# Performance work log

Measured on AMD Instinct MI355X. Metric: run time of the kernel, lower is better.

Reference implementation:

```python
import jax, jax.numpy as jnp
import numpy as np

NUM_EMBEDDINGS = 1024
EMBEDDING_DIM = 256
COMMITMENT_COST = 0.25


def setup_inputs() -> dict:
    key = jax.random.key(0)
    k1, k2 = jax.random.split(key)
    inputs = jax.random.normal(k1, (64, 32, 32, EMBEDDING_DIM), dtype=jnp.float32)
    embed = jax.random.normal(k2, (NUM_EMBEDDINGS, EMBEDDING_DIM), dtype=jnp.float32)
    return {"inputs": inputs, "embed": embed}


def reference(inputs, embed):
    # Eval-mode forward (no EMA buffer mutation), use_ema=True loss branch.
    input_shape = inputs.shape
    flat = inputs.reshape(-1, EMBEDDING_DIM)  # [N, d]
    distances = (
        jnp.sum(flat * flat, axis=1, keepdims=True)
        + jnp.sum(embed * embed, axis=1)
        - 2.0 * jnp.matmul(flat, embed.T)
    )
    encoding_indices = jnp.argmin(distances, axis=1)  # [N]
    # Gather codebook rows (equivalent to one-hot @ embed)
    quantized = embed[encoding_indices].reshape(input_shape)
    # use_ema branch: loss = commitment * mse(stop_grad(quantized), inputs)
    e_latent_loss = jnp.mean((jax.lax.stop_gradient(quantized) - inputs) ** 2)
    loss = COMMITMENT_COST * e_latent_loss
    # Straight-through estimator
    quantized_st = inputs + jax.lax.stop_gradient(quantized - inputs)
    # Perplexity from code usage histogram (== mean of one-hot encodings)
    n_tokens = flat.shape[0]
    counts = jax.ops.segment_sum(
        jnp.ones((n_tokens,), dtype=jnp.float32), encoding_indices,
        num_segments=NUM_EMBEDDINGS)
    avg_probs = counts / n_tokens
    perplexity = jnp.exp(-jnp.sum(avg_probs * jnp.log(avg_probs + 1e-10)))
    return quantized_st, loss, perplexity, encoding_indices
```

## Files before the change

kernel.cpp:

```cpp
#include <hip/hip_runtime.h>

#define NTOK 65536
#define DIM 256
#define KC 1024
#define EPS 0.08f

typedef __attribute__((ext_vector_type(8))) _Float16 f16x8;
typedef __attribute__((ext_vector_type(8))) unsigned short u16x8;
typedef __attribute__((ext_vector_type(4))) float f32x4;

static __device__ __forceinline__ unsigned short f16bits(float f) {
  _Float16 h = (_Float16)f;
  return __builtin_bit_cast(unsigned short, h);
}

#define VWAIT(n) asm volatile("s_waitcnt vmcnt(" #n ")" ::: "memory")
#define SB() __builtin_amdgcn_sched_barrier(0)
#define GLDX4(dst, p, off) \
  asm volatile("global_load_dwordx4 %0, %1, off offset:" #off \
               : "=v"(dst) : "v"(p) : "memory")

__global__ __launch_bounds__(256) void vq_prep_e(const float* __restrict__ e,
                                                 unsigned short* __restrict__ eg,
                                                 float* __restrict__ esq,
                                                 int* __restrict__ hist,
                                                 int* __restrict__ fixCount) {
  const int gid = blockIdx.x * 256 + threadIdx.x;
  const int t = gid >> 5;
  const int o = gid & 31;
  const float4 v0 = *reinterpret_cast<const float4*>(&e[t * DIM + o * 8]);
  const float4 v1 = *reinterpret_cast<const float4*>(&e[t * DIM + o * 8 + 4]);
  u16x8 u;
  u[0] = f16bits(v0.x); u[1] = f16bits(v0.y); u[2] = f16bits(v0.z); u[3] = f16bits(v0.w);
  u[4] = f16bits(v1.x); u[5] = f16bits(v1.y); u[6] = f16bits(v1.z); u[7] = f16bits(v1.w);
  const int ctk = t >> 6, njj = (t >> 4) & 3, col = t & 15;
  const int s = o >> 2, kq = o & 3;
  char* dst = (char*)eg + ((ctk * 32 + s * 4 + njj) << 10) + ((kq * 16 + col) << 4);
  *reinterpret_cast<u16x8*>(dst) = u;
  float p = v0.x * v0.x + v0.y * v0.y + v0.z * v0.z + v0.w * v0.w +
            v1.x * v1.x + v1.y * v1.y + v1.z * v1.z + v1.w * v1.w;
#pragma unroll
  for (int m = 16; m > 0; m >>= 1) p += __shfl_xor(p, m, 64);
  if (o == 0) esq[t] = p;
  if (blockIdx.x < 4) hist[blockIdx.x * 256 + threadIdx.x] = 0;
  if (gid == 0) *fixCount = 0;
}

__global__ __launch_bounds__(256, 2) void vq_argmin(
    const float* __restrict__ x, const unsigned short* __restrict__ eg,
    const float* __restrict__ esq, const float* __restrict__ e,
    float* __restrict__ outIdxF, float* __restrict__ outQ,
    float* __restrict__ bestDist, float* __restrict__ xsq,
    int* __restrict__ hist, int* __restrict__ fixCount,
    unsigned int* __restrict__ fixList) {
  const int lane = threadIdx.x & 63, w = threadIdx.x >> 6;
  const int col = lane & 15, kq = lane >> 4;
  const int tw = blockIdx.x * 128 + w * 32;

  f16x8 a[2][8];
  float sqm[2] = {0.f, 0.f};
#pragma unroll
  for (int mi = 0; mi < 2; ++mi) {
#pragma unroll
    for (int s = 0; s < 8; ++s) {
      const float* xp = &x[(tw + mi * 16 + col) * DIM + s * 32 + kq * 8];
      const float4 v0 = *reinterpret_cast<const float4*>(xp);
      const float4 v1 = *reinterpret_cast<const float4*>(xp + 4);
      a[mi][s][0] = (_Float16)v0.x; a[mi][s][1] = (_Float16)v0.y;
      a[mi][s][2] = (_Float16)v0.z; a[mi][s][3] = (_Float16)v0.w;
      a[mi][s][4] = (_Float16)v1.x; a[mi][s][5] = (_Float16)v1.y;
      a[mi][s][6] = (_Float16)v1.z; a[mi][s][7] = (_Float16)v1.w;
      sqm[mi] += v0.x * v0.x + v0.y * v0.y + v0.z * v0.z + v0.w * v0.w +
                 v1.x * v1.x + v1.y * v1.y + v1.z * v1.z + v1.w * v1.w;
    }
  }
#pragma unroll
  for (int mi = 0; mi < 2; ++mi) {
    sqm[mi] += __shfl_xor(sqm[mi], 16, 64);
    sqm[mi] += __shfl_xor(sqm[mi], 32, 64);
  }
  if (lane < 16) {
    xsq[tw + lane] = sqm[0];
    xsq[tw + 16 + lane] = sqm[1];
  }

  float v1_[2][4], v2_[2][4], v3_[2][4];
  int i1_[2][4], i2_[2][4];
#pragma unroll
  for (int mi = 0; mi < 2; ++mi)
#pragma unroll
    for (int r = 0; r < 4; ++r) {
      v1_[mi][r] = 3.4e38f; v2_[mi][r] = 3.4e38f; v3_[mi][r] = 3.4e38f;
      i1_[mi][r] = 0; i2_[mi][r] = 0;
    }

  f32x4 acc[2][4];
  f16x8 B[4][4];
  const char* p = (const char*)eg + lane * 16;

  VWAIT(0);
  SB();
#pragma unroll
  for (int g = 0; g < 4; ++g) {
    GLDX4(B[g][0], p, 0); GLDX4(B[g][1], p, 1024);
    GLDX4(B[g][2], p, 2048); GLDX4(B[g][3], p, 3072);
    p += 4096;
  }

#define STEP_BODY(S, BUF)                                                     \
  do {                                                                        \
    acc[0][0] = __builtin_amdgcn_mfma_f32_16x16x32_f16(a[0][(S)], BUF[0], acc[0][0], 0, 0, 0); \
    acc[0][1] = __builtin_amdgcn_mfma_f32_16x16x32_f16(a[0][(S)], BUF[1], acc[0][1], 0, 0, 0); \
    acc[0][2] = __builtin_amdgcn_mfma_f32_16x16x32_f16(a[0][(S)], BUF[2], acc[0][2], 0, 0, 0); \
    acc[0][3] = __builtin_amdgcn_mfma_f32_16x16x32_f16(a[0][(S)], BUF[3], acc[0][3], 0, 0, 0); \
    acc[1][0] = __builtin_amdgcn_mfma_f32_16x16x32_f16(a[1][(S)], BUF[0], acc[1][0], 0, 0, 0); \
    acc[1][1] = __builtin_amdgcn_mfma_f32_16x16x32_f16(a[1][(S)], BUF[1], acc[1][1], 0, 0, 0); \
    acc[1][2] = __builtin_amdgcn_mfma_f32_16x16x32_f16(a[1][(S)], BUF[2], acc[1][2], 0, 0, 0); \
    acc[1][3] = __builtin_amdgcn_mfma_f32_16x16x32_f16(a[1][(S)], BUF[3], acc[1][3], 0, 0, 0); \
  } while (0)

#define ISSUE(BUF)                                                 \
  do {                                                             \
    GLDX4(BUF[0], p, 0); GLDX4(BUF[1], p, 1024);                   \
    GLDX4(BUF[2], p, 2048); GLDX4(BUF[3], p, 3072);                \
    p += 4096;                                                     \
  } while (0)

#define EPILOGUE(CTK)                                                         \
  do {                                                                        \
    const float* pe = &esq[(CTK) * 64 + col];                                 \
    _Pragma("unroll") for (int njj = 0; njj < 4; ++njj) {                     \
      const int code = (CTK) * 64 + njj * 16 + col;                           \
      const float sqv = pe[njj * 16];                                         \
      _Pragma("unroll") for (int mi = 0; mi < 2; ++mi)                        \
      _Pragma("unroll") for (int r = 0; r < 4; ++r) {                         \
        const float d = fmaf(-2.f, acc[mi][njj][r], sqv);                     \
        if (d < v1_[mi][r]) {                                                 \
          v3_[mi][r] = v2_[mi][r]; v2_[mi][r] = v1_[mi][r];                   \
          i2_[mi][r] = i1_[mi][r];                                            \
          v1_[mi][r] = d; i1_[mi][r] = code;                                  \
        } else if (d < v2_[mi][r]) {                                          \
          v3_[mi][r] = v2_[mi][r]; v2_[mi][r] = d; i2_[mi][r] = code;         \
        } else if (d < v3_[mi][r]) {                                          \
          v3_[mi][r] = d;                                                     \
        }                                                                     \
      }                                                                       \
    }                                                                         \
  } while (0)

  for (int ctk = 0; ctk < 15; ++ctk) {
#pragma unroll
    for (int mi = 0; mi < 2; ++mi)
#pragma unroll
      for (int nj = 0; nj < 4; ++nj) acc[mi][nj] = (f32x4){0.f, 0.f, 0.f, 0.f};
#pragma unroll
    for (int s = 0; s < 8; ++s) {
      VWAIT(12);
      SB();
      if ((s & 3) == 0) { STEP_BODY(s, B[0]); ISSUE(B[0]); }
      else if ((s & 3) == 1) { STEP_BODY(s, B[1]); ISSUE(B[1]); }
      else if ((s & 3) == 2) { STEP_BODY(s, B[2]); ISSUE(B[2]); }
      else { STEP_BODY(s, B[3]); ISSUE(B[3]); }
    }
    EPILOGUE(ctk);
  }
  {
#pragma unroll
    for (int mi = 0; mi < 2; ++mi)
#pragma unroll
      for (int nj = 0; nj < 4; ++nj) acc[mi][nj] = (f32x4){0.f, 0.f, 0.f, 0.f};
    VWAIT(12); SB(); STEP_BODY(0, B[0]); ISSUE(B[0]);
    VWAIT(12); SB(); STEP_BODY(1, B[1]); ISSUE(B[1]);
    VWAIT(12); SB(); STEP_BODY(2, B[2]); ISSUE(B[2]);
    VWAIT(12); SB(); STEP_BODY(3, B[3]); ISSUE(B[3]);
    VWAIT(12); SB(); STEP_BODY(4, B[0]);
    VWAIT(8);  SB(); STEP_BODY(5, B[1]);
    VWAIT(4);  SB(); STEP_BODY(6, B[2]);
    VWAIT(0);  SB(); STEP_BODY(7, B[3]);
    EPILOGUE(15);
  }
#undef STEP_BODY
#undef ISSUE
#undef EPILOGUE

#pragma unroll
  for (int mi = 0; mi < 2; ++mi)
#pragma unroll
    for (int r = 0; r < 4; ++r) {
      float mv1 = v1_[mi][r], mv2 = v2_[mi][r], mv3 = v3_[mi][r];
      int mi1 = i1_[mi][r], mi2 = i2_[mi][r];
#pragma unroll
      for (int m = 1; m <= 8; m <<= 1) {
        const float ov1 = __shfl_xor(mv1, m, 64);
        const float ov2 = __shfl_xor(mv2, m, 64);
        const float ov3 = __shfl_xor(mv3, m, 64);
        const int oi1 = __shfl_xor(mi1, m, 64);
        const int oi2 = __shfl_xor(mi2, m, 64);
        const bool oW = (ov1 < mv1) || (ov1 == mv1 && oi1 < mi1);
        const float wv1 = oW ? ov1 : mv1, wv2 = oW ? ov2 : mv2, wv3 = oW ? ov3 : mv3;
        const int wi1 = oW ? oi1 : mi1, wi2 = oW ? oi2 : mi2;
        const float lv1 = oW ? mv1 : ov1, lv2 = oW ? mv2 : ov2;
        const int li1 = oW ? mi1 : oi1;
        const bool w2 = (wv2 < lv1) || (wv2 == lv1 && wi2 < li1);
        mv1 = wv1; mi1 = wi1;
        mv2 = w2 ? wv2 : lv1;
        mi2 = w2 ? wi2 : li1;
        mv3 = w2 ? fminf(wv3, lv1) : fminf(wv2, lv2);
      }
      if (col == 0) {
        const int t = tw + mi * 16 + kq * 4 + r;
        outIdxF[t] = (float)mi1;
        bestDist[t] = mv1;
        atomicAdd(&hist[mi1], 1);
        if (mv2 - mv1 < EPS) {
          const unsigned full = (mv3 - mv1 < EPS) ? 0x80000000u : 0u;
          const int pp = atomicAdd(fixCount, 1);
          fixList[pp * 2] = (unsigned)t | full;
          fixList[pp * 2 + 1] = (unsigned)mi2;
        }
      }
      i1_[mi][r] = mi1;
    }

#pragma unroll
  for (int i = 0; i < 32; ++i) {
    const int id = __shfl(i1_[i >> 4][i & 3], ((i >> 2) & 3) * 16, 64);
    const float4 q = reinterpret_cast<const float4*>(&e[id * DIM])[lane];
    reinterpret_cast<float4*>(&outQ[(tw + i) * DIM])[lane] = q;
  }
}

__global__ __launch_bounds__(256) void vq_fixup(
    const float* __restrict__ x, const float* __restrict__ e,
    const int* __restrict__ fixCount, const unsigned int* __restrict__ fixList,
    float* __restrict__ outIdxF, float* __restrict__ outQ,
    float* __restrict__ bestDist, int* __restrict__ hist) {
  const int n = *fixCount;
  const int tid = threadIdx.x;
  __shared__ float xrow[256];
  __shared__ float rv[4];
  __shared__ int ri[4];
  __shared__ int sOld, sFi;
  for (int it = blockIdx.x; it < n; it += gridDim.x) {
    const unsigned e0 = fixList[it * 2];
    const int t = (int)(e0 & 0x3FFFFFFFu);
    const bool full = (e0 >> 31) != 0u;
    if (!full) {
      if (tid < 64) {
        const int i1 = (int)outIdxF[t];
        const int i2 = (int)fixList[it * 2 + 1];
        const float4 xv = reinterpret_cast<const float4*>(&x[t * DIM])[tid];
        const float4 e1 = reinterpret_cast<const float4*>(&e[i1 * DIM])[tid];
        const float4 e2 = reinterpret_cast<const float4*>(&e[i2 * DIM])[tid];
        float d1 = (xv.x - e1.x) * (xv.x - e1.x) + (xv.y - e1.y) * (xv.y - e1.y) +
                   (xv.z - e1.z) * (xv.z - e1.z) + (xv.w - e1.w) * (xv.w - e1.w);
        float d2 = (xv.x - e2.x) * (xv.x - e2.x) + (xv.y - e2.y) * (xv.y - e2.y) +
                   (xv.z - e2.z) * (xv.z - e2.z) + (xv.w - e2.w) * (xv.w - e2.w);
#pragma unroll
        for (int m = 32; m > 0; m >>= 1) {
          d1 += __shfl_xor(d1, m, 64);
          d2 += __shfl_xor(d2, m, 64);
        }
        const bool swap2 = (d2 < d1) || (d2 == d1 && i2 < i1);
        const int wIdx = swap2 ? i2 : i1;
        const float wD = swap2 ? d2 : d1;
        if (tid == 0) {
          bestDist[t] = wD;
          if (wIdx != i1) {
            atomicSub(&hist[i1], 1);
            atomicAdd(&hist[wIdx], 1);
            outIdxF[t] = (float)wIdx;
          }
        }
        if (swap2) {
          const float4 q = reinterpret_cast<const float4*>(&e[wIdx * DIM])[tid];
          reinterpret_cast<float4*>(&outQ[t * DIM])[tid] = q;
        }
      }
    } else {
      __syncthreads();
      if (tid < 64) ((float4*)xrow)[tid] = ((const float4*)&x[t * DIM])[tid];
      __syncthreads();
      float bv = 3.4e38f; int bi = 0;
      for (int c = tid; c < KC; c += 256) {
        float s = 0.f;
#pragma unroll
        for (int d = 0; d < DIM; d += 4) {
          const float4 ev = *(const float4*)&e[c * DIM + d];
          const float d0 = xrow[d] - ev.x, d1 = xrow[d + 1] - ev.y;
          const float d2 = xrow[d + 2] - ev.z, d3 = xrow[d + 3] - ev.w;
          s += d0 * d0 + d1 * d1 + d2 * d2 + d3 * d3;
        }
        if (s < bv) { bv = s; bi = c; }
      }
#pragma unroll
      for (int m = 1; m <= 32; m <<= 1) {
        const float ob = __shfl_xor(bv, m, 64);
        const int oi = __shfl_xor(bi, m, 64);
        if (ob < bv || (ob == bv && oi < bi)) { bv = ob; bi = oi; }
      }
      const int lane = tid & 63, wv = tid >> 6;
      if (lane == 0) { rv[wv] = bv; ri[wv] = bi; }
      __syncthreads();
      if (tid == 0) {
        float fb = rv[0]; int fi = ri[0];
        for (int k = 1; k < 4; ++k)
          if (rv[k] < fb || (rv[k] == fb && ri[k] < fi)) { fb = rv[k]; fi = ri[k]; }
        sOld = (int)outIdxF[t];
        sFi = fi;
        bestDist[t] = fb;
        if (fi != sOld) {
          atomicSub(&hist[sOld], 1);
          atomicAdd(&hist[fi], 1);
          outIdxF[t] = (float)fi;
        }
      }
      __syncthreads();
      if (sFi != sOld) outQ[t * DIM + tid] = e[sFi * DIM + tid];
      __syncthreads();
    }
  }
}

__global__ __launch_bounds__(1024) void vq_final(
    const int* __restrict__ hist, const float* __restrict__ xsq,
    const float* __restrict__ bestDist, float* __restrict__ outLoss,
    float* __restrict__ outPerp) {
  const int tid = threadIdx.x;
  float ls = 0.f;
  for (int i = 0; i < 64; ++i) {
    const int t = tid + i * 1024;
    ls += xsq[t] + bestDist[t];
  }
  const float p = (float)hist[tid] * (1.f / 65536.f);
  float ent = p * logf(p + 1e-10f);
#pragma unroll
  for (int o = 32; o > 0; o >>= 1) {
    ls += __shfl_down(ls, o, 64);
    ent += __shfl_down(ent, o, 64);
  }
  __shared__ float lbuf[16], ebuf[16];
  const int lane = tid & 63, wv = tid >> 6;
  if (lane == 0) { lbuf[wv] = ls; ebuf[wv] = ent; }
  __syncthreads();
  if (tid == 0) {
    float L = 0.f, E = 0.f;
    for (int i = 0; i < 16; ++i) { L += lbuf[i]; E += ebuf[i]; }
    *outLoss = 0.25f * (L / 16777216.f);
    *outPerp = expf(-E);
  }
}

extern "C" void kernel_launch(void* const* d_in, const int* in_sizes, int n_in,
                              void* d_out, int out_size, void* d_ws, size_t ws_size,
                              hipStream_t stream) {
  const float* x = (const float*)d_in[0];
  const float* e = (const float*)d_in[1];
  float* out = (float*)d_out;
  float* outQ = out;
  float* outLoss = out + 16777216;
  float* outPerp = out + 16777217;
  float* outIdxF = out + 16777218;

  char* ws = (char*)d_ws;
  int*   hist     = (int*)ws;
  float* esq      = (float*)(ws + 4096);
  float* xsq      = (float*)(ws + 8192);
  float* bestDist = (float*)(ws + 270336);
  int*   fixCount = (int*)(ws + 532480);
  unsigned int* fixList = (unsigned int*)(ws + 532496);
  unsigned short* e_f16 = (unsigned short*)(ws + 1056784);

  vq_prep_e<<<128, 256, 0, stream>>>(e, e_f16, esq, hist, fixCount);
  vq_argmin<<<NTOK / 128, 256, 0, stream>>>(x, e_f16, esq, e, outIdxF, outQ,
                                            bestDist, xsq, hist, fixCount, fixList);
  vq_fixup<<<256, 256, 0, stream>>>(x, e, fixCount, fixList, outIdxF, outQ,
                                    bestDist, hist);
  vq_final<<<1, 1024, 0, stream>>>(hist, xsq, bestDist, outLoss, outPerp);
}
```

Before: 164.9 us.

## Stage codebook tiles through LDS with async global_load_lds triple buffering

```diff
diff --git a/kernel.cpp b/kernel.cpp
--- a/kernel.cpp
+++ b/kernel.cpp
@@ -13,12 +13,11 @@
   _Float16 h = (_Float16)f;
   return __builtin_bit_cast(unsigned short, h);
 }
-
-#define VWAIT(n) asm volatile("s_waitcnt vmcnt(" #n ")" ::: "memory")
-#define SB() __builtin_amdgcn_sched_barrier(0)
-#define GLDX4(dst, p, off) \
-  asm volatile("global_load_dwordx4 %0, %1, off offset:" #off \
-               : "=v"(dst) : "v"(p) : "memory")
+static __device__ __forceinline__ void gload16(const void* g, void* l) {
+  __builtin_amdgcn_global_load_lds(
+      (const __attribute__((address_space(1))) unsigned int*)g,
+      (__attribute__((address_space(3))) unsigned int*)l, 16, 0, 0);
+}
 
 __global__ __launch_bounds__(256) void vq_prep_e(const float* __restrict__ e,
                                                  unsigned short* __restrict__ eg,
@@ -46,16 +45,27 @@
   if (gid == 0) *fixCount = 0;
 }
 
-__global__ __launch_bounds__(256, 2) void vq_argmin(
+__global__ __launch_bounds__(128, 2) void vq_argmin(
     const float* __restrict__ x, const unsigned short* __restrict__ eg,
     const float* __restrict__ esq, const float* __restrict__ e,
     float* __restrict__ outIdxF, float* __restrict__ outQ,
     float* __restrict__ bestDist, float* __restrict__ xsq,
     int* __restrict__ hist, int* __restrict__ fixCount,
     unsigned int* __restrict__ fixList) {
-  const int lane = threadIdx.x & 63, w = threadIdx.x >> 6;
+  __shared__ char esb[3 * 8192];
+  __shared__ float es_sq[KC];
+
+  const int tid = threadIdx.x;
+  const int lane = tid & 63, w = tid >> 6;
   const int col = lane & 15, kq = lane >> 4;
-  const int tw = blockIdx.x * 128 + w * 32;
+  const int tw = blockIdx.x * 64 + w * 32;
+
+  {
+    const float4* s4 = reinterpret_cast<const float4*>(esq);
+    float4* d4 = reinterpret_cast<float4*>(es_sq);
+    d4[tid * 2] = s4[tid * 2];
+    d4[tid * 2 + 1] = s4[tid * 2 + 1];
+  }
 
   f16x8 a[2][8];
   float sqm[2] = {0.f, 0.f};
@@ -84,6 +94,13 @@
     xsq[tw + 16 + lane] = sqm[1];
   }
 
+  auto STAGE = [&](int q, int b) {
+#pragma unroll
+    for (int i = 0; i < 4; ++i)
+      gload16((const char*)eg + q * 8192 + w * 4096 + i * 1024 + lane * 16,
+              esb + b * 8192 + w * 4096 + i * 1024);
+  };
+
   float v1_[2][4], v2_[2][4], v3_[2][4];
   int i1_[2][4], i2_[2][4];
 #pragma unroll
@@ -94,94 +111,66 @@
       i1_[mi][r] = 0; i2_[mi][r] = 0;
     }
 
+  STAGE(0, 0);
+
   f32x4 acc[2][4];
-  f16x8 B[4][4];
-  const char* p = (const char*)eg + lane * 16;
-
-  VWAIT(0);
-  SB();
-#pragma unroll
-  for (int g = 0; g < 4; ++g) {
-    GLDX4(B[g][0], p, 0); GLDX4(B[g][1], p, 1024);
-    GLDX4(B[g][2], p, 2048); GLDX4(B[g][3], p, 3072);
-    p += 4096;
-  }
-
-#define STEP_BODY(S, BUF)                                                     \
-  do {                                                                        \
-    acc[0][0] = __builtin_amdgcn_mfma_f32_16x16x32_f16(a[0][(S)], BUF[0], acc[0][0], 0, 0, 0); \
-    acc[0][1] = __builtin_amdgcn_mfma_f32_16x16x32_f16(a[0][(S)], BUF[1], acc[0][1], 0, 0, 0); \
-    acc[0][2] = __builtin_amdgcn_mfma_f32_16x16x32_f16(a[0][(S)], BUF[2], acc[0][2], 0, 0, 0); \
-    acc[0][3] = __builtin_amdgcn_mfma_f32_16x16x32_f16(a[0][(S)], BUF[3], acc[0][3], 0, 0, 0); \
-    acc[1][0] = __builtin_amdgcn_mfma_f32_16x16x32_f16(a[1][(S)], BUF[0], acc[1][0], 0, 0, 0); \
-    acc[1][1] = __builtin_amdgcn_mfma_f32_16x16x32_f16(a[1][(S)], BUF[1], acc[1][1], 0, 0, 0); \
-    acc[1][2] = __builtin_amdgcn_mfma_f32_16x16x32_f16(a[1][(S)], BUF[2], acc[1][2], 0, 0, 0); \
-    acc[1][3] = __builtin_amdgcn_mfma_f32_16x16x32_f16(a[1][(S)], BUF[3], acc[1][3], 0, 0, 0); \
-  } while (0)
-
-#define ISSUE(BUF)                                                 \
-  do {                                                             \
-    GLDX4(BUF[0], p, 0); GLDX4(BUF[1], p, 1024);                   \
-    GLDX4(BUF[2], p, 2048); GLDX4(BUF[3], p, 3072);                \
-    p += 4096;                                                     \
-  } while (0)
-
-#define EPILOGUE(CTK)                                                         \
-  do {                                                                        \
-    const float* pe = &esq[(CTK) * 64 + col];                                 \
-    _Pragma("unroll") for (int njj = 0; njj < 4; ++njj) {                     \
-      const int code = (CTK) * 64 + njj * 16 + col;                           \
-      const float sqv = pe[njj * 16];                                         \
-      _Pragma("unroll") for (int mi = 0; mi < 2; ++mi)                        \
-      _Pragma("unroll") for (int r = 0; r < 4; ++r) {                         \
-        const float d = fmaf(-2.f, acc[mi][njj][r], sqv);                     \
-        if (d < v1_[mi][r]) {                                                 \
-          v3_[mi][r] = v2_[mi][r]; v2_[mi][r] = v1_[mi][r];                   \
-          i2_[mi][r] = i1_[mi][r];                                            \
-          v1_[mi][r] = d; i1_[mi][r] = code;                                  \
-        } else if (d < v2_[mi][r]) {                                          \
-          v3_[mi][r] = v2_[mi][r]; v2_[mi][r] = d; i2_[mi][r] = code;         \
-        } else if (d < v3_[mi][r]) {                                          \
-          v3_[mi][r] = d;                                                     \
-        }                                                                     \
-      }                                                                       \
-    }                                                                         \
-  } while (0)
-
-  for (int ctk = 0; ctk < 15; ++ctk) {
+  for (int ctk = 0; ctk < 16; ++ctk) {
 #pragma unroll
     for (int mi = 0; mi < 2; ++mi)
 #pragma unroll
       for (int nj = 0; nj < 4; ++nj) acc[mi][nj] = (f32x4){0.f, 0.f, 0.f, 0.f};
-#pragma unroll
-    for (int s = 0; s < 8; ++s) {
-      VWAIT(12);
-      SB();
-      if ((s & 3) == 0) { STEP_BODY(s, B[0]); ISSUE(B[0]); }
-      else if ((s & 3) == 1) { STEP_BODY(s, B[1]); ISSUE(B[1]); }
-      else if ((s & 3) == 2) { STEP_BODY(s, B[2]); ISSUE(B[2]); }
-      else { STEP_BODY(s, B[3]); ISSUE(B[3]); }
-    }
-    EPILOGUE(ctk);
-  }
-  {
-#pragma unroll
-    for (int mi = 0; mi < 2; ++mi)
-#pragma unroll
-      for (int nj = 0; nj < 4; ++nj) acc[mi][nj] = (f32x4){0.f, 0.f, 0.f, 0.f};
-    VWAIT(12); SB(); STEP_BODY(0, B[0]); ISSUE(B[0]);
-    VWAIT(12); SB(); STEP_BODY(1, B[1]); ISSUE(B[1]);
-    VWAIT(12); SB(); STEP_BODY(2, B[2]); ISSUE(B[2]);
-    VWAIT(12); SB(); STEP_BODY(3, B[3]); ISSUE(B[3]);
-    VWAIT(12); SB(); STEP_BODY(4, B[0]);
-    VWAIT(8);  SB(); STEP_BODY(5, B[1]);
-    VWAIT(4);  SB(); STEP_BODY(6, B[2]);
-    VWAIT(0);  SB(); STEP_BODY(7, B[3]);
-    EPILOGUE(15);
-  }
-#undef STEP_BODY
-#undef ISSUE
-#undef EPILOGUE
+
+#pragma unroll
+    for (int ks2 = 0; ks2 < 4; ++ks2) {
+      const int q = ctk * 4 + ks2;
+      if (q < 63) {
+        STAGE(q + 1, (q + 1) % 3);
+        asm volatile("s_waitcnt vmcnt(4)" ::: "memory");
+      } else {
+        asm volatile("s_waitcnt vmcnt(0)" ::: "memory");
+      }
+      __builtin_amdgcn_s_barrier();
+      asm volatile("" ::: "memory");
+
+      const char* bb = esb + (q % 3) * 8192;
+#pragma unroll
+      for (int h = 0; h < 2; ++h) {
+        f16x8 bfr[4];
+#pragma unroll
+        for (int njj = 0; njj < 4; ++njj)
+          bfr[njj] = *reinterpret_cast<const f16x8*>(
+              bb + (h * 4 + njj) * 1024 + lane * 16);
+        const int sg = ks2 * 2 + h;
+#pragma unroll
+        for (int mi = 0; mi < 2; ++mi)
+#pragma unroll
+          for (int njj = 0; njj < 4; ++njj)
+            acc[mi][njj] = __builtin_amdgcn_mfma_f32_16x16x32_f16(
+                a[mi][sg], bfr[njj], acc[mi][njj], 0, 0, 0);
+      }
+    }
+
+#pragma unroll
+    for (int njj = 0; njj < 4; ++njj) {
+      const int code = ctk * 64 + njj * 16 + col;
+      const float sqv = es_sq[code];
+#pragma unroll
+      for (int mi = 0; mi < 2; ++mi)
+#pragma unroll
+        for (int r = 0; r < 4; ++r) {
+          const float d = fmaf(-2.f, acc[mi][njj][r], sqv);
+          if (d < v1_[mi][r]) {
+            v3_[mi][r] = v2_[mi][r]; v2_[mi][r] = v1_[mi][r];
+            i2_[mi][r] = i1_[mi][r];
+            v1_[mi][r] = d; i1_[mi][r] = code;
+          } else if (d < v2_[mi][r]) {
+            v3_[mi][r] = v2_[mi][r]; v2_[mi][r] = d; i2_[mi][r] = code;
+          } else if (d < v3_[mi][r]) {
+            v3_[mi][r] = d;
+          }
+        }
+    }
+  }
 
 #pragma unroll
   for (int mi = 0; mi < 2; ++mi)
@@ -372,8 +361,8 @@
   unsigned short* e_f16 = (unsigned short*)(ws + 1056784);
 
   vq_prep_e<<<128, 256, 0, stream>>>(e, e_f16, esq, hist, fixCount);
-  vq_argmin<<<NTOK / 128, 256, 0, stream>>>(x, e_f16, esq, e, outIdxF, outQ,
-                                            bestDist, xsq, hist, fixCount, fixList);
+  vq_argmin<<<NTOK / 64, 128, 0, stream>>>(x, e_f16, esq, e, outIdxF, outQ,
+                                           bestDist, xsq, hist, fixCount, fixList);
   vq_fixup<<<256, 256, 0, stream>>>(x, e, fixCount, fixList, outIdxF, outQ,
                                     bestDist, hist);
   vq_final<<<1, 1024, 0, stream>>>(hist, xsq, bestDist, outLoss, outPerp);
```

Result: slower. 170.3 us (+3.3%).
